# Optimization experiments

Measured on AMD Instinct MI355X. Metric: run time of the kernel, lower is better.

Reference implementation:

```python
import jax, jax.numpy as jnp
import numpy as np

B, L, C, H = 2, 2048, 2048, 16
COND = 2048
HID = 4 * C
LN_EPS = 1e-6


def _ln(x):
    m = jnp.mean(x, axis=-1, keepdims=True)
    v = jnp.mean((x - m) ** 2, axis=-1, keepdims=True)
    return (x - m) / jnp.sqrt(v + LN_EPS)


def _gelu_tanh(u):
    c = np.sqrt(2.0 / np.pi).astype(np.float32)
    return 0.5 * u * (1.0 + jnp.tanh(c * (u + 0.044715 * u ** 3)))


def setup_inputs() -> dict:
    key = jax.random.key(0)
    ks = jax.random.split(key, 8)
    s = 0.02
    return {
        "x": jax.random.normal(ks[0], (B, L, C), jnp.float32),
        "cond_BD": jax.random.normal(ks[1], (B, COND), jnp.float32),
        "attn_bias": jnp.zeros((1, 1, L, L), jnp.float32),
        "Wqkv": (jax.random.normal(ks[2], (3 * C, C), jnp.float32) * s),
        "q_bias": jnp.zeros((C,), jnp.float32),
        "v_bias": jnp.zeros((C,), jnp.float32),
        "scale_mul_log": jnp.full((1, H, 1, 1), np.log(4.0), jnp.float32),
        "Wproj": (jax.random.normal(ks[3], (C, C), jnp.float32) * s),
        "bproj": jnp.zeros((C,), jnp.float32),
        "Wada": (jax.random.normal(ks[4], (6 * C, COND), jnp.float32) * s),
        "bada": jnp.zeros((6 * C,), jnp.float32),
        "Wfc1": (jax.random.normal(ks[5], (HID, C), jnp.float32) * s),
        "bfc1": jnp.zeros((HID,), jnp.float32),
        "Wfc2": (jax.random.normal(ks[6], (C, HID), jnp.float32) * s),
        "bfc2": jnp.zeros((C,), jnp.float32),
    }


def reference(x, cond_BD, attn_bias, Wqkv, q_bias, v_bias, scale_mul_log,
              Wproj, bproj, Wada, bada, Wfc1, bfc1, Wfc2, bfc2):
    Bs, Lx, Cx = x.shape
    D = Cx // H
    # AdaLN modulation: SiLU -> Linear(cond_dim, 6C) -> view(B,1,6,C).unbind(2)
    ada = (jax.nn.silu(cond_BD) @ Wada.T + bada).reshape(Bs, 1, 6, Cx)
    gamma1, gamma2, scale1, scale2, shift1, shift2 = [ada[:, :, i, :] for i in range(6)]

    def attn(xin):
        qkv_bias = jnp.concatenate([q_bias, jnp.zeros_like(q_bias), v_bias])
        qkv = (xin @ Wqkv.T + qkv_bias).reshape(Bs, Lx, 3, H, D)
        qkv = jnp.transpose(qkv, (2, 0, 3, 1, 4))  # [3, B, H, L, D]
        q, k, v = qkv[0], qkv[1], qkv[2]
        # cos-attn: L2-normalize q,k; q scaled by exp(clamped log-scale); softmax scale = 1
        sm = jnp.exp(jnp.minimum(scale_mul_log, jnp.log(jnp.float32(100.0))))
        qn = q / jnp.maximum(jnp.linalg.norm(q, axis=-1, keepdims=True), 1e-12) * sm
        kn = k / jnp.maximum(jnp.linalg.norm(k, axis=-1, keepdims=True), 1e-12)
        scores = jnp.einsum('bhqd,bhkd->bhqk', qn, kn) + attn_bias
        p = jax.nn.softmax(scores, axis=-1)
        o = jnp.einsum('bhqk,bhkd->bhqd', p, v)
        o = jnp.transpose(o, (0, 2, 1, 3)).reshape(Bs, Lx, Cx)
        return o @ Wproj.T + bproj

    x = x + attn(_ln(x) * (scale1 + 1.0) + shift1) * gamma1
    h = _gelu_tanh((_ln(x) * (scale2 + 1.0) + shift2) @ Wfc1.T + bfc1)
    x = x + (h @ Wfc2.T + bfc2) * gamma2
    return x
```

## Files before the change

kernel.cpp:

```cpp
#include <hip/hip_runtime.h>

typedef unsigned short u16;
typedef float f32x4 __attribute__((ext_vector_type(4)));
typedef short short8 __attribute__((ext_vector_type(8)));

#define C_ 2048
#define L_ 2048
#define H_ 16
#define D_ 128
#define SIXC 12288

__device__ __forceinline__ u16 f2bf(float f) {
  union { float f; unsigned u; } v; v.f = f;
  unsigned r = v.u + 0x7FFFu + ((v.u >> 16) & 1u);
  return (u16)(r >> 16);
}
__device__ __forceinline__ float bf2f(u16 b) {
  union { unsigned u; float f; } v; v.u = ((unsigned)b) << 16; return v.f;
}

#define GLOAD_LDS16(g, l)                                            \
  __builtin_amdgcn_global_load_lds(                                  \
      (__attribute__((address_space(1))) void*)(g),                  \
      (__attribute__((address_space(3))) void*)(l), 16, 0, 0)

template <int N> __device__ __forceinline__ void wait_vmcnt() {
  if constexpr (N == 8)      asm volatile("s_waitcnt vmcnt(8)" ::: "memory");
  else if constexpr (N == 6) asm volatile("s_waitcnt vmcnt(6)" ::: "memory");
  else                       asm volatile("s_waitcnt vmcnt(0)" ::: "memory");
}

__global__ __launch_bounds__(256) void conv_bf16(
    const float* __restrict__ src, u16* __restrict__ dst, int n) {
  int i = (blockIdx.x * 256 + threadIdx.x) * 4;
  if (i >= n) return;
  float4 v = *(const float4*)&src[i];
  ushort4 o;
  o.x = f2bf(v.x); o.y = f2bf(v.y); o.z = f2bf(v.z); o.w = f2bf(v.w);
  *(ushort4*)&dst[i] = o;
}

__global__ __launch_bounds__(256) void prep_kernel(
    const float* __restrict__ cond, const float* __restrict__ qb,
    const float* __restrict__ vb, const float* __restrict__ sml,
    float* __restrict__ silu_cond, float* __restrict__ qkvbias,
    float* __restrict__ sm) {
  int i = blockIdx.x * 256 + threadIdx.x;
  if (i < 4096) { float c = cond[i]; silu_cond[i] = c / (1.f + __expf(-c)); }
  if (i < 6144) {
    float bv = (i < 2048) ? qb[i] : ((i < 4096) ? 0.f : vb[i - 4096]);
    qkvbias[i] = bv;
  }
  if (i < 16) sm[i] = __expf(fminf(sml[i], 4.6051701859880914f));
}

__global__ __launch_bounds__(256) void ada_gemm(
    const float* __restrict__ sc, const float* __restrict__ Wada,
    const float* __restrict__ bada, float* __restrict__ ada) {
  int gw = (blockIdx.x * 256 + threadIdx.x) >> 6;
  int lane = threadIdx.x & 63;
  int b = gw / SIXC, row = gw % SIXC;
  const float* s0 = sc + b * 2048;
  const float* w0 = Wada + (size_t)row * 2048;
  float s = 0.f;
  for (int k = lane * 4; k < 2048; k += 256) {
    float4 a = *(const float4*)&s0[k];
    float4 w = *(const float4*)&w0[k];
    s = fmaf(a.x, w.x, s); s = fmaf(a.y, w.y, s);
    s = fmaf(a.z, w.z, s); s = fmaf(a.w, w.w, s);
  }
  #pragma unroll
  for (int off = 32; off; off >>= 1) s += __shfl_xor(s, off);
  if (lane == 0) ada[(size_t)b * SIXC + row] = s + bada[row];
}

__global__ __launch_bounds__(256) void ln_mod(
    const float* __restrict__ x, const float* __restrict__ ada,
    u16* __restrict__ out, int soff, int shoff) {
  int r = blockIdx.x;
  int b = r >> 11;
  int tid = threadIdx.x;
  const float* xr = x + (size_t)r * 2048;
  int c0 = tid * 8;
  float4 u0 = *(const float4*)&xr[c0];
  float4 u1 = *(const float4*)&xr[c0 + 4];
  float v[8] = {u0.x,u0.y,u0.z,u0.w,u1.x,u1.y,u1.z,u1.w};
  float s = 0.f, s2 = 0.f;
  #pragma unroll
  for (int j = 0; j < 8; ++j) { s += v[j]; s2 = fmaf(v[j], v[j], s2); }
  int wv = tid >> 6, lane = tid & 63;
  #pragma unroll
  for (int off = 32; off; off >>= 1) { s += __shfl_xor(s, off); s2 += __shfl_xor(s2, off); }
  __shared__ float red[8];
  if (!lane) { red[wv] = s; red[4 + wv] = s2; }
  __syncthreads();
  s = red[0] + red[1] + red[2] + red[3];
  s2 = red[4] + red[5] + red[6] + red[7];
  float mean = s * (1.f / 2048.f);
  float var = s2 * (1.f / 2048.f) - mean * mean;
  float rstd = rsqrtf(var + 1e-6f);
  const float* sc = ada + (size_t)b * SIXC + soff;
  const float* sh = ada + (size_t)b * SIXC + shoff;
  u16* orow = out + (size_t)r * 2048;
  #pragma unroll
  for (int j = 0; j < 8; ++j) {
    int c = c0 + j;
    float y = (v[j] - mean) * rstd * (1.f + sc[c]) + sh[c];
    orow[c] = f2bf(y);
  }
}

__global__ __launch_bounds__(256) void qk_norm_bf(
    u16* __restrict__ qb, u16* __restrict__ kb, const float* __restrict__ sm) {
  int gw = (blockIdx.x * 256 + threadIdx.x) >> 6;
  int lane = threadIdx.x & 63;
  int which = gw >> 16;
  int rid = gw & 0xFFFF;
  int h = (rid >> 11) & 15;
  u16* base = (which ? kb : qb) + (size_t)rid * 128 + lane * 2;
  unsigned uu = *(const unsigned*)base;
  float v0 = bf2f((u16)(uu & 0xFFFFu));
  float v1 = bf2f((u16)(uu >> 16));
  float ss = v0 * v0 + v1 * v1;
  #pragma unroll
  for (int off = 32; off; off >>= 1) ss += __shfl_xor(ss, off);
  float rn = 1.f / fmaxf(sqrtf(ss), 1e-12f);
  if (which == 0) rn *= sm[h];
  unsigned o = (unsigned)f2bf(v0 * rn) | ((unsigned)f2bf(v1 * rn) << 16);
  *(unsigned*)base = o;
}

#define PSP 68
__global__ __launch_bounds__(256) void attn_mfma(
    const u16* __restrict__ qb, const u16* __restrict__ kb,
    const u16* __restrict__ vbt, const float* __restrict__ bias,
    u16* __restrict__ o) {
  __shared__ u16 Ks[2][64 * 128];
  __shared__ u16 Vt[2][128 * 64];
  __shared__ u16 Ps[4][16 * PSP];
  int tid = threadIdx.x;
  int w = tid >> 6, lane = tid & 63;
  int flat = blockIdx.y * gridDim.x + blockIdx.x;
  int rl = (flat & 7) * 128 + (flat >> 3);
  int bh = rl >> 5, b = bh >> 4, h = bh & 15;
  int q0 = (rl & 31) * 64;
  int lr = lane & 15, lg = lane >> 4;
  short8 aq[4];
  {
    const u16* qrow = qb + ((size_t)bh * L_ + q0 + w * 16 + lr) * 128 + lg * 8;
    #pragma unroll
    for (int ks = 0; ks < 4; ++ks) aq[ks] = *(const short8*)(qrow + ks * 32);
  }
  f32x4 oacc[8] = {};
  float m = -1e30f, l = 0.f;
  const float* brow = bias + (size_t)(q0 + w * 16 + lr) * L_;
  const u16* kbase = kb + (size_t)bh * L_ * 128;
  const u16* vbase = vbt + (size_t)bh * 128 * L_;
  const int kq0 = tid;
  const int vq0 = tid;

  float4 brg[4], bnr[4];
  #pragma unroll
  for (int i = 0; i < 4; ++i) {
    int q = i * 256 + kq0;
    int r = q >> 4, c = q & 15;
    GLOAD_LDS16(kbase + (size_t)r * 128 + ((c ^ (r & 7)) * 8), &Ks[0][q * 8]);
  }
  #pragma unroll
  for (int i = 0; i < 4; ++i) {
    int q = i * 256 + vq0;
    int r = q >> 3, c = q & 7;
    GLOAD_LDS16(vbase + (size_t)r * L_ + ((c ^ (r & 7)) * 8), &Vt[0][q * 8]);
  }
  #pragma unroll
  for (int kg = 0; kg < 4; ++kg)
    brg[kg] = *(const float4*)&brow[kg * 16 + lg * 4];
  __syncthreads();

  for (int kt = 0; kt < 32; ++kt) {
    const int cur = kt & 1;
    if (kt < 31) {
      const int nxt = cur ^ 1;
      const u16* kb2 = kbase + (size_t)(kt + 1) * 64 * 128;
      #pragma unroll
      for (int i = 0; i < 4; ++i) {
        int q = i * 256 + kq0;
        int r = q >> 4, c = q & 15;
        GLOAD_LDS16(kb2 + (size_t)r * 128 + ((c ^ (r & 7)) * 8), &Ks[nxt][q * 8]);
      }
      #pragma unroll
      for (int i = 0; i < 4; ++i) {
        int q = i * 256 + vq0;
        int r = q >> 3, c = q & 7;
        GLOAD_LDS16(vbase + (size_t)r * L_ + (kt + 1) * 64 + ((c ^ (r & 7)) * 8),
                    &Vt[nxt][q * 8]);
      }
      #pragma unroll
      for (int kg = 0; kg < 4; ++kg)
        bnr[kg] = *(const float4*)&brow[(kt + 1) * 64 + kg * 16 + lg * 4];
    }
    f32x4 s[4] = {};
    __builtin_amdgcn_s_setprio(1);
    #pragma unroll
    for (int ks = 0; ks < 4; ++ks) {
      #pragma unroll
      for (int kg = 0; kg < 4; ++kg) {
        int row = kg * 16 + lr;
        short8 bk = *(const short8*)&Ks[cur][row * 128 + (((ks * 4 + lg) ^ (lr & 7)) * 8)];
        s[kg] = __builtin_amdgcn_mfma_f32_16x16x32_bf16(bk, aq[ks], s[kg], 0, 0, 0);
      }
    }
    __builtin_amdgcn_s_setprio(0);
    float p[4][4];
    #pragma unroll
    for (int kg = 0; kg < 4; ++kg) {
      p[kg][0] = s[kg][0] + brg[kg].x;
      p[kg][1] = s[kg][1] + brg[kg].y;
      p[kg][2] = s[kg][2] + brg[kg].z;
      p[kg][3] = s[kg][3] + brg[kg].w;
    }
    float tm = fmaxf(
        fmaxf(fmaxf(fmaxf(p[0][0], p[0][1]), fmaxf(p[0][2], p[0][3])),
              fmaxf(fmaxf(p[1][0], p[1][1]), fmaxf(p[1][2], p[1][3]))),
        fmaxf(fmaxf(fmaxf(p[2][0], p[2][1]), fmaxf(p[2][2], p[2][3])),
              fmaxf(fmaxf(p[3][0], p[3][1]), fmaxf(p[3][2], p[3][3]))));
    tm = fmaxf(tm, __shfl_xor(tm, 16));
    tm = fmaxf(tm, __shfl_xor(tm, 32));
    if (__any(tm > m + 8.f)) {
      float nm = fmaxf(m, tm);
      float a = __expf(m - nm);
      m = nm;
      l *= a;
      float al[4];
      #pragma unroll
      for (int j = 0; j < 4; ++j) al[j] = __shfl(a, lg * 4 + j);
      #pragma unroll
      for (int dg = 0; dg < 8; ++dg) {
        f32x4 t = oacc[dg];
        t[0] *= al[0]; t[1] *= al[1]; t[2] *= al[2]; t[3] *= al[3];
        oacc[dg] = t;
      }
    }
    float ps = 0.f;
    #pragma unroll
    for (int kg = 0; kg < 4; ++kg) {
      #pragma unroll
      for (int j = 0; j < 4; ++j) { p[kg][j] = __expf(p[kg][j] - m); ps += p[kg][j]; }
    }
    ps += __shfl_xor(ps, 16);
    ps += __shfl_xor(ps, 32);
    l += ps;
    #pragma unroll
    for (int kg = 0; kg < 4; ++kg) {
      unsigned lo = (unsigned)f2bf(p[kg][0]) | ((unsigned)f2bf(p[kg][1]) << 16);
      unsigned hi = (unsigned)f2bf(p[kg][2]) | ((unsigned)f2bf(p[kg][3]) << 16);
      uint2 w2; w2.x = lo; w2.y = hi;
      *(uint2*)&Ps[w][lr * PSP + kg * 16 + lg * 4] = w2;
    }
    __threadfence_block();
    short8 pa0 = *(const short8*)&Ps[w][lr * PSP + lg * 8];
    short8 pa1 = *(const short8*)&Ps[w][lr * PSP + 32 + lg * 8];
    __builtin_amdgcn_s_setprio(1);
    #pragma unroll
    for (int dg = 0; dg < 8; ++dg) {
      int row = dg * 16 + lr;
      short8 bv0 = *(const short8*)&Vt[cur][row * 64 + ((lg ^ (lr & 7)) * 8)];
      oacc[dg] = __builtin_amdgcn_mfma_f32_16x16x32_bf16(pa0, bv0, oacc[dg], 0, 0, 0);
      short8 bv1 = *(const short8*)&Vt[cur][row * 64 + (((4 + lg) ^ (lr & 7)) * 8)];
      oacc[dg] = __builtin_amdgcn_mfma_f32_16x16x32_bf16(pa1, bv1, oacc[dg], 0, 0, 0);
    }
    __builtin_amdgcn_s_setprio(0);
    __syncthreads();
    #pragma unroll
    for (int i = 0; i < 4; ++i) brg[i] = bnr[i];
  }
  float inv[4];
  #pragma unroll
  for (int j = 0; j < 4; ++j) inv[j] = 1.f / __shfl(l, lg * 4 + j);
  #pragma unroll
  for (int j = 0; j < 4; ++j) {
    u16* dst = &o[((size_t)(b * L_) + q0 + w * 16 + lg * 4 + j) * 2048 + h * 128 + lr];
    #pragma unroll
    for (int dg = 0; dg < 8; ++dg) dst[dg * 16] = f2bf(oacc[dg][j] * inv[j]);
  }
}

#define RD_A(cur, mh)                                                         \
  _Pragma("unroll") for (int kk = 0; kk < 2; ++kk) {                          \
    const int col_ = (kk * 32 + lg * 8) ^ cswz;                               \
    _Pragma("unroll") for (int i = 0; i < 4; ++i)                             \
      af[i][kk] = *(const short8*)                                            \
          &As[cur][(wr * 128 + (mh) * 64 + i * 16 + lr) * 64 + col_];         \
  }
#define RD_B(cur, nh, BB)                                                     \
  _Pragma("unroll") for (int kk = 0; kk < 2; ++kk) {                          \
    const int col_ = (kk * 32 + lg * 8) ^ cswz;                               \
    _Pragma("unroll") for (int j = 0; j < 2; ++j)                             \
      BB[j][kk] = *(const short8*)                                            \
          &Bs[cur][(wc * 64 + (nh) * 32 + j * 16 + lr) * 64 + col_];          \
  }
#define MMQ(mh, nh, BB)                                                       \
  __builtin_amdgcn_s_setprio(1);                                              \
  _Pragma("unroll") for (int kk = 0; kk < 2; ++kk)                            \
  _Pragma("unroll") for (int i = 0; i < 4; ++i)                               \
  _Pragma("unroll") for (int j = 0; j < 2; ++j)                               \
    acc[(mh) * 4 + i][(nh) * 2 + j] = __builtin_amdgcn_mfma_f32_16x16x32_bf16(\
        af[i][kk], BB[j][kk], acc[(mh) * 4 + i][(nh) * 2 + j], 0, 0, 0);      \
  __builtin_amdgcn_s_setprio(0);
#define LGKM0 asm volatile("s_waitcnt lgkmcnt(0)" ::: "memory")

template <int EPI>
__global__ __launch_bounds__(512, 2) void gemm256(
    const u16* __restrict__ A, const u16* __restrict__ W,
    const float* __restrict__ bias,
    u16* __restrict__ outb,
    u16* __restrict__ p0, u16* __restrict__ p1, u16* __restrict__ p2,
    int M, int N, int K, int lda) {
  __shared__ __attribute__((aligned(16))) u16 As[2][256 * 64];
  __shared__ __attribute__((aligned(16))) u16 Bs[2][256 * 64];
  const int tid = threadIdx.x;
  int my = blockIdx.y, half = 0;
  if constexpr (EPI == 3) { half = my >> 4; my &= 15; }
  const int m0 = my * 256, n0 = blockIdx.x * 256;
  const int wv = tid >> 6, lane = tid & 63;
  const int wr = wv >> 2, wc = wv & 3;
  const int lr = lane & 15, lg = lane >> 4;
  const int sr = lane >> 3;
  const int scol = ((lane & 7) ^ sr) * 8;
  const int cswz = (lr & 7) * 8;
  f32x4 acc[8][4] = {};
  const u16* Ab = A + (size_t)m0 * lda + (size_t)half * K;
  const u16* Bb = W + (size_t)n0 * lda + (size_t)half * K;
  const int nt = K >> 6;

  auto stA2 = [&](int bi, int k0, int sel) {
    #pragma unroll
    for (int q = 0; q < 2; ++q) {
      int c = wv * 2 + q;
      int chunk = sel == 0 ? (c < 8 ? c : c + 8)
                           : (c < 8 ? c + 8 : c + 16);
      int row = chunk * 8 + sr;
      GLOAD_LDS16(Ab + (size_t)row * lda + k0 + scol, &As[bi][chunk * 512]);
    }
  };
  auto stA4 = [&](int bi, int k0) {
    #pragma unroll
    for (int q = 0; q < 4; ++q) {
      int chunk = wv * 4 + q, row = chunk * 8 + sr;
      GLOAD_LDS16(Ab + (size_t)row * lda + k0 + scol, &As[bi][chunk * 512]);
    }
  };
  auto stB4 = [&](int bi, int k0) {
    #pragma unroll
    for (int q = 0; q < 4; ++q) {
      int chunk = wv * 4 + q, row = chunk * 8 + sr;
      GLOAD_LDS16(Bb + (size_t)row * lda + k0 + scol, &Bs[bi][chunk * 512]);
    }
  };

  short8 af[4][2], bfl[2][2], bfh[2][2];
  stA4(0, 0); stB4(0, 0);
  stA4(1, 64); stB4(1, 64);
  wait_vmcnt<8>();
  __builtin_amdgcn_s_barrier();

  for (int t = 0; t < nt; ++t) {
    const int cur = t & 1;
    const int k2 = (t + 2) << 6;
    const bool st = t + 2 < nt;
    RD_A(cur, 0); RD_B(cur, 0, bfl);
    __builtin_amdgcn_s_barrier();
    LGKM0;
    MMQ(0, 0, bfl);
    __builtin_amdgcn_s_barrier();
    RD_B(cur, 1, bfh);
    __builtin_amdgcn_s_barrier();
    LGKM0;
    if (st) stA2(cur, k2, 0);
    MMQ(0, 1, bfh);
    __builtin_amdgcn_s_barrier();
    RD_A(cur, 1);
    __builtin_amdgcn_s_barrier();
    LGKM0;
    if (st) stB4(cur, k2);
    MMQ(1, 0, bfl);
    __builtin_amdgcn_s_barrier();
    __builtin_amdgcn_sched_barrier(0x10F);
    if (st) { stA2(cur, k2, 1); wait_vmcnt<8>(); }
    else if (t + 1 < nt) { wait_vmcnt<0>(); }
    MMQ(1, 1, bfh);
    __builtin_amdgcn_s_barrier();
  }

  #pragma unroll
  for (int mi = 0; mi < 8; ++mi) {
    #pragma unroll
    for (int ni = 0; ni < 4; ++ni) {
      int gcol = n0 + wc * 64 + ni * 16 + lr;
      float bv = (EPI == 3) ? 0.f : bias[gcol];
      #pragma unroll
      for (int j = 0; j < 4; ++j) {
        int grow = m0 + wr * 128 + mi * 16 + lg * 4 + j;
        float v = acc[mi][ni][j] + bv;
        if constexpr (EPI == 0) {
          int which = gcol >> 11;
          int h = (gcol >> 7) & 15;
          int d = gcol & 127;
          int b = grow >> 11, ll = grow & 2047;
          int bh = b * 16 + h;
          if (which == 0)      p0[((size_t)bh * L_ + ll) * 128 + d] = f2bf(v);
          else if (which == 1) p1[((size_t)bh * L_ + ll) * 128 + d] = f2bf(v);
          else                 p2[((size_t)bh * 128 + d) * L_ + ll] = f2bf(v);
        } else if constexpr (EPI == 1) {
          float u = 0.7978845608028654f * (v + 0.044715f * v * v * v);
          float e = __expf(2.f * u);
          float th = 1.f - 2.f / (e + 1.f);
          outb[(size_t)grow * N + gcol] = f2bf(0.5f * v * (1.f + th));
        } else {
          u16* pd = half ? p1 : p0;
          pd[(size_t)grow * N + gcol] = f2bf(v);
        }
      }
    }
  }
}

__global__ __launch_bounds__(256) void fc2_combine(
    const u16* __restrict__ pa, const u16* __restrict__ pb,
    const float* __restrict__ bias, const float* __restrict__ res,
    const float* __restrict__ ada, float* __restrict__ out) {
  int i = (blockIdx.x * 256 + threadIdx.x) * 4;
  int col = i & 2047;
  int b = i >> 22;
  ushort4 a4 = *(const ushort4*)&pa[i];
  ushort4 b4 = *(const ushort4*)&pb[i];
  float4 r = *(const float4*)&res[i];
  const float* ad = ada + (size_t)b * SIXC + C_;
  float4 o;
  o.x = r.x + (bf2f(a4.x) + bf2f(b4.x) + bias[col])     * ad[col];
  o.y = r.y + (bf2f(a4.y) + bf2f(b4.y) + bias[col + 1]) * ad[col + 1];
  o.z = r.z + (bf2f(a4.z) + bf2f(b4.z) + bias[col + 2]) * ad[col + 2];
  o.w = r.w + (bf2f(a4.w) + bf2f(b4.w) + bias[col + 3]) * ad[col + 3];
  *(float4*)&out[i] = o;
}

template <int EPI>
__global__ __launch_bounds__(256) void gemm128(
    const u16* __restrict__ A, const u16* __restrict__ W,
    const float* __restrict__ bias, const float* __restrict__ res,
    const float* __restrict__ ada, int goff,
    float* __restrict__ outf, u16* __restrict__ outb,
    int M, int N, int K) {
  __shared__ u16 As[2][128 * 64];
  __shared__ u16 Bs[2][128 * 64];
  const int tid = threadIdx.x;
  const int m0 = blockIdx.y * 128, n0 = blockIdx.x * 128;
  const int wv = tid >> 6, lane = tid & 63;
  const int wr = wv >> 1, wc = wv & 1;
  const int lr = lane & 15, lg = lane >> 4;
  const int sr = lane >> 3;
  const int scol = ((lane & 7) ^ sr) * 8;
  const int cswz = (lr & 7) * 8;
  f32x4 acc[4][4] = {};
  const u16* Ab = A + (size_t)m0 * K;
  const u16* Bb = W + (size_t)n0 * K;
  const int nt = K >> 6;
  auto stage = [&](int bi, int k0) {
    #pragma unroll
    for (int p = 0; p < 4; ++p) {
      int chunk = wv * 4 + p;
      int row = chunk * 8 + sr;
      GLOAD_LDS16(Ab + (size_t)row * K + k0 + scol, &As[bi][chunk * 512]);
      GLOAD_LDS16(Bb + (size_t)row * K + k0 + scol, &Bs[bi][chunk * 512]);
    }
  };
  stage(0, 0);
  stage(1, 64);
  for (int t = 0; t < nt; ++t) {
    const int cur = t & 1;
    if (t + 1 < nt) wait_vmcnt<8>(); else wait_vmcnt<0>();
    __builtin_amdgcn_s_barrier();
    __builtin_amdgcn_sched_barrier(0);
    #pragma unroll
    for (int kk = 0; kk < 2; ++kk) {
      short8 af[4], bfr[4];
      const int col = (kk * 32 + lg * 8) ^ cswz;
      #pragma unroll
      for (int i = 0; i < 4; ++i) {
        af[i]  = *(const short8*)&As[cur][(wr * 64 + i * 16 + lr) * 64 + col];
        bfr[i] = *(const short8*)&Bs[cur][(wc * 64 + i * 16 + lr) * 64 + col];
      }
      #pragma unroll
      for (int mi = 0; mi < 4; ++mi)
        #pragma unroll
        for (int ni = 0; ni < 4; ++ni)
          acc[mi][ni] = __builtin_amdgcn_mfma_f32_16x16x32_bf16(af[mi], bfr[ni], acc[mi][ni], 0, 0, 0);
    }
    __builtin_amdgcn_sched_barrier(0);
    asm volatile("s_waitcnt lgkmcnt(0)" ::: "memory");
    __builtin_amdgcn_s_barrier();
    __builtin_amdgcn_sched_barrier(0);
    if (t + 2 < nt) stage(cur, (t + 2) << 6);
  }
  #pragma unroll
  for (int mi = 0; mi < 4; ++mi) {
    #pragma unroll
    for (int ni = 0; ni < 4; ++ni) {
      int gcol = n0 + wc * 64 + ni * 16 + lr;
      float bv = bias[gcol];
      #pragma unroll
      for (int j = 0; j < 4; ++j) {
        int grow = m0 + wr * 64 + mi * 16 + lg * 4 + j;
        float v = acc[mi][ni][j] + bv;
        if (EPI == 1) {
          float u = 0.7978845608028654f * (v + 0.044715f * v * v * v);
          float e = __expf(2.f * u);
          float th = 1.f - 2.f / (e + 1.f);
          outb[(size_t)grow * N + gcol] = f2bf(0.5f * v * (1.f + th));
        } else {
          int b = grow >> 11;
          float g = ada[(size_t)b * SIXC + goff + gcol];
          size_t oi = (size_t)grow * N + gcol;
          outf[oi] = res[oi] + v * g;
        }
      }
    }
  }
}

extern "C" void kernel_launch(void* const* d_in, const int* in_sizes, int n_in,
                              void* d_out, int out_size, void* d_ws, size_t ws_size,
                              hipStream_t stream) {
  const float* x        = (const float*)d_in[0];
  const float* cond     = (const float*)d_in[1];
  const float* attnbias = (const float*)d_in[2];
  const float* Wqkv     = (const float*)d_in[3];
  const float* q_bias   = (const float*)d_in[4];
  const float* v_bias   = (const float*)d_in[5];
  const float* sml      = (const float*)d_in[6];
  const float* Wproj    = (const float*)d_in[7];
  const float* bproj    = (const float*)d_in[8];
  const float* Wada     = (const float*)d_in[9];
  const float* bada     = (const float*)d_in[10];
  const float* bfc1     = (const float*)d_in[12];
  const float* Wfc1     = (const float*)d_in[11];
  const float* Wfc2     = (const float*)d_in[13];
  const float* bfc2     = (const float*)d_in[14];
  float* out = (float*)d_out;
  char* ws = (char*)d_ws;
  const size_t MB = 1ull << 20;

  float* silu_cond = (float*)(ws + 0);
  float* qkvbias   = (float*)(ws + (16 << 10));
  float* smbuf     = (float*)(ws + (40 << 10));
  float* adab      = (float*)(ws + (48 << 10));
  u16*   xob       = (u16*)(ws + 1 * MB);
  u16*   qbb       = (u16*)(ws + 17 * MB);
  u16*   kbb       = (u16*)(ws + 33 * MB);
  float* x1        = (float*)(ws + 17 * MB);
  u16*   vbt       = (u16*)(ws + 49 * MB);
  u16*   hbuf      = (u16*)(ws + 49 * MB);
  u16*   wqkv_bf   = (u16*)(ws + 65 * MB);
  u16*   wproj_bf  = (u16*)(ws + 89 * MB);
  u16*   wfc1_bf   = (u16*)(ws + 113 * MB);
  u16*   wfc2_bf   = (u16*)(ws + 145 * MB);
  u16*   pa        = (u16*)(ws + 1 * MB);
  u16*   pb        = (u16*)(ws + 113 * MB);

  conv_bf16<<<12288, 256, 0, stream>>>(Wqkv, wqkv_bf, 6144 * 2048);
  conv_bf16<<<4096, 256, 0, stream>>>(Wproj, wproj_bf, 2048 * 2048);
  conv_bf16<<<16384, 256, 0, stream>>>(Wfc1, wfc1_bf, 8192 * 2048);
  conv_bf16<<<16384, 256, 0, stream>>>(Wfc2, wfc2_bf, 2048 * 8192);
  prep_kernel<<<24, 256, 0, stream>>>(cond, q_bias, v_bias, sml, silu_cond, qkvbias, smbuf);
  ada_gemm<<<6144, 256, 0, stream>>>(silu_cond, Wada, bada, adab);
  ln_mod<<<4096, 256, 0, stream>>>(x, adab, xob, 2 * C_, 4 * C_);
  gemm256<0><<<dim3(24, 16), 512, 0, stream>>>(xob, wqkv_bf, qkvbias,
      nullptr, qbb, kbb, vbt, 4096, 6144, 2048, 2048);
  qk_norm_bf<<<32768, 256, 0, stream>>>(qbb, kbb, smbuf);
  attn_mfma<<<dim3(32, 32), 256, 0, stream>>>(qbb, kbb, vbt, attnbias, xob);
  gemm128<2><<<dim3(16, 32), 256, 0, stream>>>(xob, wproj_bf, bproj, x, adab, 0,
      x1, nullptr, 4096, 2048, 2048);
  ln_mod<<<4096, 256, 0, stream>>>(x1, adab, xob, 3 * C_, 5 * C_);
  gemm256<1><<<dim3(32, 16), 512, 0, stream>>>(xob, wfc1_bf, bfc1,
      hbuf, nullptr, nullptr, nullptr, 4096, 8192, 2048, 2048);
  gemm256<3><<<dim3(8, 32), 512, 0, stream>>>(hbuf, wfc2_bf, bfc2,
      nullptr, pa, pb, nullptr, 4096, 2048, 4096, 8192);
  fc2_combine<<<8192, 256, 0, stream>>>(pa, pb, bfc2, x1, adab, out);
}
```

Baseline: 778.8 us.

## Replace 256x256 GEMM with 256x128 tile, K=32 double-buffered simple pipeline

Replaces the large-tile GEMM (256x256 tile, 512 threads, K-step 64, finely interleaved stage/MFMA schedule) with a 256x128 tile on 256 threads using a K-step of 32 and a plain double-buffered loop. Each wave now computes a 128x64 sub-tile and reads its full fragments once per K-step. Grids double in the N dimension for the QKV, FC1 and FC2 GEMMs. The change gives up the hand-interleaved load/compute overlap and some operand reuse in exchange for more blocks, lower LDS use and a simpler schedule. The combine kernel is renamed and takes the gamma offset as a parameter.

```diff
diff --git a/kernel.cpp b/kernel.cpp
--- a/kernel.cpp
+++ b/kernel.cpp
@@ -285,111 +285,70 @@
   }
 }
 
-#define RD_A(cur, mh)                                                         \
-  _Pragma("unroll") for (int kk = 0; kk < 2; ++kk) {                          \
-    const int col_ = (kk * 32 + lg * 8) ^ cswz;                               \
-    _Pragma("unroll") for (int i = 0; i < 4; ++i)                             \
-      af[i][kk] = *(const short8*)                                            \
-          &As[cur][(wr * 128 + (mh) * 64 + i * 16 + lr) * 64 + col_];         \
-  }
-#define RD_B(cur, nh, BB)                                                     \
-  _Pragma("unroll") for (int kk = 0; kk < 2; ++kk) {                          \
-    const int col_ = (kk * 32 + lg * 8) ^ cswz;                               \
-    _Pragma("unroll") for (int j = 0; j < 2; ++j)                             \
-      BB[j][kk] = *(const short8*)                                            \
-          &Bs[cur][(wc * 64 + (nh) * 32 + j * 16 + lr) * 64 + col_];          \
-  }
-#define MMQ(mh, nh, BB)                                                       \
-  __builtin_amdgcn_s_setprio(1);                                              \
-  _Pragma("unroll") for (int kk = 0; kk < 2; ++kk)                            \
-  _Pragma("unroll") for (int i = 0; i < 4; ++i)                               \
-  _Pragma("unroll") for (int j = 0; j < 2; ++j)                               \
-    acc[(mh) * 4 + i][(nh) * 2 + j] = __builtin_amdgcn_mfma_f32_16x16x32_bf16(\
-        af[i][kk], BB[j][kk], acc[(mh) * 4 + i][(nh) * 2 + j], 0, 0, 0);      \
-  __builtin_amdgcn_s_setprio(0);
-#define LGKM0 asm volatile("s_waitcnt lgkmcnt(0)" ::: "memory")
-
 template <int EPI>
-__global__ __launch_bounds__(512, 2) void gemm256(
+__global__ __launch_bounds__(256, 2) void gemm_mn(
     const u16* __restrict__ A, const u16* __restrict__ W,
     const float* __restrict__ bias,
     u16* __restrict__ outb,
     u16* __restrict__ p0, u16* __restrict__ p1, u16* __restrict__ p2,
     int M, int N, int K, int lda) {
-  __shared__ __attribute__((aligned(16))) u16 As[2][256 * 64];
-  __shared__ __attribute__((aligned(16))) u16 Bs[2][256 * 64];
+  __shared__ __attribute__((aligned(16))) u16 As[2][256 * 32];
+  __shared__ __attribute__((aligned(16))) u16 Bs[2][128 * 32];
   const int tid = threadIdx.x;
   int my = blockIdx.y, half = 0;
   if constexpr (EPI == 3) { half = my >> 4; my &= 15; }
-  const int m0 = my * 256, n0 = blockIdx.x * 256;
+  const int m0 = my * 256, n0 = blockIdx.x * 128;
   const int wv = tid >> 6, lane = tid & 63;
-  const int wr = wv >> 2, wc = wv & 3;
+  const int wr = wv >> 1, wc = wv & 1;
   const int lr = lane & 15, lg = lane >> 4;
-  const int sr = lane >> 3;
-  const int scol = ((lane & 7) ^ sr) * 8;
-  const int cswz = (lr & 7) * 8;
+  const int srow = lane >> 2;
+  const int gcolst = (((lane & 3) ^ ((lane >> 2) & 3)) * 8);
+  const int cswz = (lr & 3) * 8 | 0;
   f32x4 acc[8][4] = {};
   const u16* Ab = A + (size_t)m0 * lda + (size_t)half * K;
   const u16* Bb = W + (size_t)n0 * lda + (size_t)half * K;
-  const int nt = K >> 6;
-
-  auto stA2 = [&](int bi, int k0, int sel) {
-    #pragma unroll
-    for (int q = 0; q < 2; ++q) {
-      int c = wv * 2 + q;
-      int chunk = sel == 0 ? (c < 8 ? c : c + 8)
-                           : (c < 8 ? c + 8 : c + 16);
-      int row = chunk * 8 + sr;
-      GLOAD_LDS16(Ab + (size_t)row * lda + k0 + scol, &As[bi][chunk * 512]);
+  const int nt = K >> 5;
+
+  auto stage = [&](int bi, int k0) {
+    #pragma unroll
+    for (int p = 0; p < 4; ++p) {
+      int chunk = wv * 4 + p;
+      int row = chunk * 16 + srow;
+      GLOAD_LDS16(Ab + (size_t)row * lda + k0 + gcolst, &As[bi][chunk * 512]);
+    }
+    #pragma unroll
+    for (int p = 0; p < 2; ++p) {
+      int chunk = wv * 2 + p;
+      int row = chunk * 16 + srow;
+      GLOAD_LDS16(Bb + (size_t)row * lda + k0 + gcolst, &Bs[bi][chunk * 512]);
     }
   };
-  auto stA4 = [&](int bi, int k0) {
-    #pragma unroll
-    for (int q = 0; q < 4; ++q) {
-      int chunk = wv * 4 + q, row = chunk * 8 + sr;
-      GLOAD_LDS16(Ab + (size_t)row * lda + k0 + scol, &As[bi][chunk * 512]);
-    }
-  };
-  auto stB4 = [&](int bi, int k0) {
-    #pragma unroll
-    for (int q = 0; q < 4; ++q) {
-      int chunk = wv * 4 + q, row = chunk * 8 + sr;
-      GLOAD_LDS16(Bb + (size_t)row * lda + k0 + scol, &Bs[bi][chunk * 512]);
-    }
-  };
-
-  short8 af[4][2], bfl[2][2], bfh[2][2];
-  stA4(0, 0); stB4(0, 0);
-  stA4(1, 64); stB4(1, 64);
-  wait_vmcnt<8>();
-  __builtin_amdgcn_s_barrier();
-
+
+  stage(0, 0);
+  stage(1, 32);
   for (int t = 0; t < nt; ++t) {
     const int cur = t & 1;
-    const int k2 = (t + 2) << 6;
-    const bool st = t + 2 < nt;
-    RD_A(cur, 0); RD_B(cur, 0, bfl);
+    if (t + 1 < nt) wait_vmcnt<6>(); else wait_vmcnt<0>();
     __builtin_amdgcn_s_barrier();
-    LGKM0;
-    MMQ(0, 0, bfl);
+    __builtin_amdgcn_sched_barrier(0);
+    short8 af[8], bf[4];
+    const int col = (lg * 8) ^ cswz;
+    #pragma unroll
+    for (int i = 0; i < 8; ++i)
+      af[i] = *(const short8*)&As[cur][(wr * 128 + i * 16 + lr) * 32 + col];
+    #pragma unroll
+    for (int j = 0; j < 4; ++j)
+      bf[j] = *(const short8*)&Bs[cur][(wc * 64 + j * 16 + lr) * 32 + col];
+    #pragma unroll
+    for (int i = 0; i < 8; ++i)
+      #pragma unroll
+      for (int j = 0; j < 4; ++j)
+        acc[i][j] = __builtin_amdgcn_mfma_f32_16x16x32_bf16(af[i], bf[j], acc[i][j], 0, 0, 0);
+    __builtin_amdgcn_sched_barrier(0);
+    asm volatile("s_waitcnt lgkmcnt(0)" ::: "memory");
     __builtin_amdgcn_s_barrier();
-    RD_B(cur, 1, bfh);
-    __builtin_amdgcn_s_barrier();
-    LGKM0;
-    if (st) stA2(cur, k2, 0);
-    MMQ(0, 1, bfh);
-    __builtin_amdgcn_s_barrier();
-    RD_A(cur, 1);
-    __builtin_amdgcn_s_barrier();
-    LGKM0;
-    if (st) stB4(cur, k2);
-    MMQ(1, 0, bfl);
-    __builtin_amdgcn_s_barrier();
-    __builtin_amdgcn_sched_barrier(0x10F);
-    if (st) { stA2(cur, k2, 1); wait_vmcnt<8>(); }
-    else if (t + 1 < nt) { wait_vmcnt<0>(); }
-    MMQ(1, 1, bfh);
-    __builtin_amdgcn_s_barrier();
+    __builtin_amdgcn_sched_barrier(0);
+    if (t + 2 < nt) stage(cur, (t + 2) << 5);
   }
 
   #pragma unroll
@@ -425,17 +384,17 @@
   }
 }
 
-__global__ __launch_bounds__(256) void fc2_combine(
+__global__ __launch_bounds__(256) void sk_combine(
     const u16* __restrict__ pa, const u16* __restrict__ pb,
     const float* __restrict__ bias, const float* __restrict__ res,
-    const float* __restrict__ ada, float* __restrict__ out) {
+    const float* __restrict__ ada, int goff, float* __restrict__ out) {
   int i = (blockIdx.x * 256 + threadIdx.x) * 4;
   int col = i & 2047;
   int b = i >> 22;
   ushort4 a4 = *(const ushort4*)&pa[i];
   ushort4 b4 = *(const ushort4*)&pb[i];
   float4 r = *(const float4*)&res[i];
-  const float* ad = ada + (size_t)b * SIXC + C_;
+  const float* ad = ada + (size_t)b * SIXC + goff;
   float4 o;
   o.x = r.x + (bf2f(a4.x) + bf2f(b4.x) + bias[col])     * ad[col];
   o.y = r.y + (bf2f(a4.y) + bf2f(b4.y) + bias[col + 1]) * ad[col + 1];
@@ -542,8 +501,8 @@
   const float* bproj    = (const float*)d_in[8];
   const float* Wada     = (const float*)d_in[9];
   const float* bada     = (const float*)d_in[10];
+  const float* Wfc1     = (const float*)d_in[11];
   const float* bfc1     = (const float*)d_in[12];
-  const float* Wfc1     = (const float*)d_in[11];
   const float* Wfc2     = (const float*)d_in[13];
   const float* bfc2     = (const float*)d_in[14];
   float* out = (float*)d_out;
@@ -574,16 +533,16 @@
   prep_kernel<<<24, 256, 0, stream>>>(cond, q_bias, v_bias, sml, silu_cond, qkvbias, smbuf);
   ada_gemm<<<6144, 256, 0, stream>>>(silu_cond, Wada, bada, adab);
   ln_mod<<<4096, 256, 0, stream>>>(x, adab, xob, 2 * C_, 4 * C_);
-  gemm256<0><<<dim3(24, 16), 512, 0, stream>>>(xob, wqkv_bf, qkvbias,
+  gemm_mn<0><<<dim3(48, 16), 256, 0, stream>>>(xob, wqkv_bf, qkvbias,
       nullptr, qbb, kbb, vbt, 4096, 6144, 2048, 2048);
   qk_norm_bf<<<32768, 256, 0, stream>>>(qbb, kbb, smbuf);
   attn_mfma<<<dim3(32, 32), 256, 0, stream>>>(qbb, kbb, vbt, attnbias, xob);
   gemm128<2><<<dim3(16, 32), 256, 0, stream>>>(xob, wproj_bf, bproj, x, adab, 0,
       x1, nullptr, 4096, 2048, 2048);
   ln_mod<<<4096, 256, 0, stream>>>(x1, adab, xob, 3 * C_, 5 * C_);
-  gemm256<1><<<dim3(32, 16), 512, 0, stream>>>(xob, wfc1_bf, bfc1,
+  gemm_mn<1><<<dim3(64, 16), 256, 0, stream>>>(xob, wfc1_bf, bfc1,
       hbuf, nullptr, nullptr, nullptr, 4096, 8192, 2048, 2048);
-  gemm256<3><<<dim3(8, 32), 512, 0, stream>>>(hbuf, wfc2_bf, bfc2,
+  gemm_mn<3><<<dim3(16, 32), 256, 0, stream>>>(hbuf, wfc2_bf, bfc2,
       nullptr, pa, pb, nullptr, 4096, 2048, 4096, 8192);
-  fc2_combine<<<8192, 256, 0, stream>>>(pa, pb, bfc2, x1, adab, out);
-}
+  sk_combine<<<8192, 256, 0, stream>>>(pa, pb, bfc2, x1, adab, C_, out);
+}
```

Measured after the change: 821.1 us. 1.05x slower.
